# Performance work log

Hardware: AMD Instinct MI355X
Metric: run time of the kernel (lower is better)

The kernel has to match this reference:

```python
import jax, jax.numpy as jnp
import numpy as np

B, S, D = 4, 4096, 1024
H, EXPAND, DCONV = 8, 2, 4
DI = D * EXPAND           # d_inner = 2048
HD = DI // H              # head_dim = 256
LN_EPS = 1e-5


def setup_inputs() -> dict:
    key = jax.random.key(0)
    ks = jax.random.split(key, 6)
    scale = lambda fan_in: 1.0 / np.sqrt(fan_in)
    return {
        "x": jax.random.normal(ks[0], (B, S, D), dtype=jnp.float32),
        "norm_w": jnp.ones((D,), dtype=jnp.float32),
        "norm_b": jnp.zeros((D,), dtype=jnp.float32),
        "in_proj_w": jax.random.normal(ks[1], (2 * DI, D), dtype=jnp.float32) * scale(D),
        "conv_w": jax.random.normal(ks[2], (DI, 1, DCONV), dtype=jnp.float32) * scale(DCONV),
        "conv_b": jax.random.normal(ks[3], (DI,), dtype=jnp.float32) * 0.02,
        "out_proj_w": jax.random.normal(ks[4], (D, DI), dtype=jnp.float32) * scale(DI),
        "log_alpha": jax.random.uniform(ks[5], (H,), dtype=jnp.float32,
                                        minval=np.log(0.1), maxval=np.log(0.99)),
    }


def reference(x, norm_w, norm_b, in_proj_w, conv_w, conv_b, out_proj_w, log_alpha):
    residual = x
    # LayerNorm
    mu = jnp.mean(x, axis=-1, keepdims=True)
    var = jnp.var(x, axis=-1, keepdims=True)
    xn = (x - mu) * jax.lax.rsqrt(var + LN_EPS) * norm_w + norm_b
    # input projection -> [B, S, 2*DI]
    xz = jnp.einsum("bsd,ed->bse", xn, in_proj_w)
    x_path, gate = xz[..., :DI], xz[..., DI:]
    # causal depthwise conv1d (torch pads d_conv-1 both sides then slices [:S])
    kernel = jnp.transpose(conv_w, (2, 1, 0))  # [DCONV, 1, DI] (WIO)
    x_path = jax.lax.conv_general_dilated(
        x_path, kernel, window_strides=(1,), padding=[(DCONV - 1, 0)],
        dimension_numbers=("NWC", "WIO", "NWC"), feature_group_count=DI,
    ) + conv_b
    # multi-head scalar-decay linear recurrence: y_t = alpha*y_{t-1} + x_t
    xh = x_path.reshape(B, S, H, HD)
    alpha = jax.nn.sigmoid(log_alpha)[:, None]  # [H, 1]

    def step(y, xt):
        y = alpha * y + xt
        return y, y

    y0 = jnp.zeros((B, H, HD), dtype=x.dtype)
    _, ys = jax.lax.scan(step, y0, jnp.transpose(xh, (1, 0, 2, 3)))  # [S, B, H, HD]
    x_path = jnp.transpose(ys, (1, 0, 2, 3)).reshape(B, S, DI)
    # gate + output projection (dropout in eval mode = identity)
    x_path = jax.nn.silu(x_path) * gate
    out = jnp.einsum("bse,de->bsd", x_path, out_proj_w)
    return out + residual
```

## Files before the change

kernel.cpp:

```cpp
#include <hip/hip_runtime.h>
#include <hip/hip_bf16.h>
#include <cstdint>

#define Bb 4
#define Ss 4096
#define Dd 1024
#define Hh 8
#define DI 2048
#define HD 256
#define XZN 4096
#define Mtot 16384
#define NCH 128
#define CHUNK 32

typedef __bf16 bf16_t;
typedef __bf16 bf16x8 __attribute__((ext_vector_type(8)));
typedef __bf16 bf16x4 __attribute__((ext_vector_type(4)));
typedef float f32x4 __attribute__((ext_vector_type(4)));

__device__ __forceinline__ float sigmoidf_(float x) { return 1.f / (1.f + __expf(-x)); }

__device__ __forceinline__ void async_ld16(void* lds, const void* g) {
  __builtin_amdgcn_global_load_lds(
      (const __attribute__((address_space(1))) void*)(uintptr_t)g,
      (__attribute__((address_space(3))) void*)(uint32_t)(uintptr_t)lds,
      16, 0, 0);
}

__global__ __launch_bounds__(256) void cvt_kernel(const float* __restrict__ s,
                                                  bf16_t* __restrict__ d) {
  const int i = blockIdx.x * 256 + threadIdx.x;
  const float4 v = ((const float4*)s)[i];
  bf16_t* o = d + 4 * (size_t)i;
  o[0] = (bf16_t)v.x; o[1] = (bf16_t)v.y; o[2] = (bf16_t)v.z; o[3] = (bf16_t)v.w;
}

__global__ __launch_bounds__(256) void ln_kernel(const float* __restrict__ x,
                                                 const float* __restrict__ w,
                                                 const float* __restrict__ b,
                                                 bf16_t* __restrict__ xn) {
  __shared__ float red[8];
  const int row = blockIdx.x;
  const float4 v = ((const float4*)(x + (size_t)row * Dd))[threadIdx.x];
  float s  = v.x + v.y + v.z + v.w;
  float s2 = v.x * v.x + v.y * v.y + v.z * v.z + v.w * v.w;
  #pragma unroll
  for (int off = 32; off; off >>= 1) { s += __shfl_down(s, off); s2 += __shfl_down(s2, off); }
  const int wave = threadIdx.x >> 6, lane = threadIdx.x & 63;
  if (lane == 0) { red[wave * 2] = s; red[wave * 2 + 1] = s2; }
  __syncthreads();
  if (threadIdx.x == 0) {
    float S = 0.f, S2 = 0.f;
    for (int i = 0; i < 4; ++i) { S += red[i * 2]; S2 += red[i * 2 + 1]; }
    red[0] = S; red[1] = S2;
  }
  __syncthreads();
  const float mean = red[0] * (1.f / Dd);
  const float var  = red[1] * (1.f / Dd) - mean * mean;
  const float rstd = rsqrtf(var + 1e-5f);
  const float4 wv = ((const float4*)w)[threadIdx.x];
  const float4 bv = ((const float4*)b)[threadIdx.x];
  bf16_t* o = xn + (size_t)row * Dd + threadIdx.x * 4;
  o[0] = (bf16_t)((v.x - mean) * rstd * wv.x + bv.x);
  o[1] = (bf16_t)((v.y - mean) * rstd * wv.y + bv.y);
  o[2] = (bf16_t)((v.z - mean) * rstd * wv.z + bv.z);
  o[3] = (bf16_t)((v.w - mean) * rstd * wv.w + bv.w);
}

template <int ADD_RES, int MINW>
__global__ __launch_bounds__(256, MINW) void gemm_bt(const bf16_t* __restrict__ A,
                                                     const bf16_t* __restrict__ Bw,
                                                     void* __restrict__ Cv,
                                                     const float* __restrict__ res,
                                                     int M, int N, int K) {
  __shared__ __align__(16) bf16_t As[128 * 64];
  __shared__ __align__(16) bf16_t Bs[128 * 64];
  const int tid = threadIdx.x;
  const int wave = tid >> 6, lane = tid & 63;
  const int bm = blockIdx.y, bn = blockIdx.x;
  const int waveM = (wave >> 1) << 6;
  const int waveN = (wave & 1) << 6;

  f32x4 acc[4][4];
  #pragma unroll
  for (int i = 0; i < 4; ++i)
    #pragma unroll
    for (int j = 0; j < 4; ++j) acc[i][j] = (f32x4){0.f, 0.f, 0.f, 0.f};

  const int pr = lane >> 3;
  const int cg = (lane & 7) ^ pr;
  const bf16_t* Ag = A + (size_t)(bm * 128 + pr) * K + cg * 8;
  const bf16_t* Bg = Bw + (size_t)(bn * 128 + pr) * K + cg * 8;

  const int fr = lane & 15;
  const int fq = lane >> 4;

  for (int kt = 0; kt < K; kt += 64) {
    #pragma unroll
    for (int i = 0; i < 4; ++i) {
      const int ii = wave * 4 + i;
      async_ld16(&As[ii * 512], Ag + (size_t)(ii * 8) * K + kt);
      async_ld16(&Bs[ii * 512], Bg + (size_t)(ii * 8) * K + kt);
    }
    __syncthreads();
    #pragma unroll
    for (int ks = 0; ks < 2; ++ks) {
      bf16x8 af[4], bfv[4];
      #pragma unroll
      for (int mt = 0; mt < 4; ++mt) {
        const int row = waveM + mt * 16 + fr;
        const int p = (ks * 4 + fq) ^ (row & 7);
        af[mt] = *(const bf16x8*)&As[row * 64 + p * 8];
      }
      #pragma unroll
      for (int nt = 0; nt < 4; ++nt) {
        const int row = waveN + nt * 16 + fr;
        const int p = (ks * 4 + fq) ^ (row & 7);
        bfv[nt] = *(const bf16x8*)&Bs[row * 64 + p * 8];
      }
      #pragma unroll
      for (int mt = 0; mt < 4; ++mt)
        #pragma unroll
        for (int nt = 0; nt < 4; ++nt)
          acc[mt][nt] =
              __builtin_amdgcn_mfma_f32_16x16x32_bf16(af[mt], bfv[nt], acc[mt][nt], 0, 0, 0);
    }
    __syncthreads();
  }

  const int n0 = bn * 128 + waveN + fr;
  const int m0 = bm * 128 + waveM + fq * 4;
  #pragma unroll
  for (int mt = 0; mt < 4; ++mt)
    #pragma unroll
    for (int nt = 0; nt < 4; ++nt)
      #pragma unroll
      for (int r = 0; r < 4; ++r) {
        const size_t m = (size_t)(m0 + mt * 16 + r);
        const size_t n = (size_t)(n0 + nt * 16);
        if (ADD_RES)
          ((float*)Cv)[m * N + n] = acc[mt][nt][r] + res[m * N + n];
        else
          ((bf16_t*)Cv)[m * N + n] = (bf16_t)acc[mt][nt][r];
      }
}

__global__ __launch_bounds__(256) void scanA_kernel(const bf16_t* __restrict__ xz,
                                                    const float* __restrict__ conv_w,
                                                    const float* __restrict__ conv_b,
                                                    const float* __restrict__ log_alpha,
                                                    float* __restrict__ carry) {
  const int half  = blockIdx.x & 1;
  const int chunk = (blockIdx.x >> 1) & (NCH - 1);
  const int b     = blockIdx.x >> 8;
  const int ch    = half * 1024 + threadIdx.x * 4;
  const float alpha = sigmoidf_(log_alpha[ch >> 8]);
  float w[4][4], bias[4];
  #pragma unroll
  for (int j = 0; j < 4; ++j) {
    const float4 cw = ((const float4*)conv_w)[ch + j];
    w[j][0] = cw.x; w[j][1] = cw.y; w[j][2] = cw.z; w[j][3] = cw.w;
    bias[j] = conv_b[ch + j];
  }
  const int s0 = chunk * CHUNK;
  const size_t base = ((size_t)b * Ss + s0) * XZN + ch;
  float x3[4] = {0,0,0,0}, x2[4] = {0,0,0,0}, x1[4] = {0,0,0,0}, y[4] = {0,0,0,0};
  if (chunk > 0) {
    const bf16x4 v3 = *(const bf16x4*)(xz + base - 3 * (size_t)XZN);
    const bf16x4 v2 = *(const bf16x4*)(xz + base - 2 * (size_t)XZN);
    const bf16x4 v1 = *(const bf16x4*)(xz + base - 1 * (size_t)XZN);
    #pragma unroll
    for (int j = 0; j < 4; ++j) { x3[j] = (float)v3[j]; x2[j] = (float)v2[j]; x1[j] = (float)v1[j]; }
  }
  #pragma unroll 4
  for (int t = 0; t < CHUNK; ++t) {
    const bf16x4 v = *(const bf16x4*)(xz + base + (size_t)t * XZN);
    #pragma unroll
    for (int j = 0; j < 4; ++j) {
      const float xc = (float)v[j];
      const float cv = bias[j] + w[j][0] * x3[j] + w[j][1] * x2[j] + w[j][2] * x1[j] + w[j][3] * xc;
      x3[j] = x2[j]; x2[j] = x1[j]; x1[j] = xc;
      y[j] = fmaf(alpha, y[j], cv);
    }
  }
  *(float4*)(carry + ((size_t)b * NCH + chunk) * DI + ch) =
      make_float4(y[0], y[1], y[2], y[3]);
}

__global__ __launch_bounds__(256) void scanB_kernel(const float* __restrict__ carry,
                                                    float* __restrict__ carryin,
                                                    const float* __restrict__ log_alpha) {
  __shared__ float S[8][32];
  const int b   = blockIdx.x >> 6;
  const int chg = blockIdx.x & 63;
  const int cg  = threadIdx.x >> 5;
  const int chl = threadIdx.x & 31;
  const int ch  = chg * 32 + chl;
  const float alpha = sigmoidf_(log_alpha[ch >> 8]);
  const float lal  = log2f(alpha);
  const float aL   = exp2f((float)CHUNK * lal);
  const float aL16 = exp2f((float)(CHUNK * 16) * lal);
  const size_t base = ((size_t)b * NCH + cg * 16) * DI + ch;
  float v[16];
  #pragma unroll
  for (int i = 0; i < 16; ++i) v[i] = carry[base + (size_t)i * DI];
  float Sl = v[0];
  #pragma unroll
  for (int i = 1; i < 16; ++i) Sl = fmaf(aL, Sl, v[i]);
  S[cg][chl] = Sl;
  __syncthreads();
  float P = 0.f;
  for (int h = 0; h < cg; ++h) P = fmaf(aL16, P, S[h][chl]);
  #pragma unroll
  for (int i = 0; i < 16; ++i) {
    carryin[base + (size_t)i * DI] = P;
    P = fmaf(aL, P, v[i]);
  }
}

__global__ __launch_bounds__(256) void scanC_kernel(const bf16_t* __restrict__ xz,
                                                    const float* __restrict__ conv_w,
                                                    const float* __restrict__ conv_b,
                                                    const float* __restrict__ log_alpha,
                                                    const float* __restrict__ carryin,
                                                    bf16_t* __restrict__ act) {
  const int half  = blockIdx.x & 1;
  const int chunk = (blockIdx.x >> 1) & (NCH - 1);
  const int b     = blockIdx.x >> 8;
  const int ch    = half * 1024 + threadIdx.x * 4;
  const float alpha = sigmoidf_(log_alpha[ch >> 8]);
  float w[4][4], bias[4];
  #pragma unroll
  for (int j = 0; j < 4; ++j) {
    const float4 cw = ((const float4*)conv_w)[ch + j];
    w[j][0] = cw.x; w[j][1] = cw.y; w[j][2] = cw.z; w[j][3] = cw.w;
    bias[j] = conv_b[ch + j];
  }
  const int s0 = chunk * CHUNK;
  const size_t base = ((size_t)b * Ss + s0) * XZN + ch;
  float x3[4] = {0,0,0,0}, x2[4] = {0,0,0,0}, x1[4] = {0,0,0,0}, y[4];
  const float4 cin = *(const float4*)(carryin + ((size_t)b * NCH + chunk) * DI + ch);
  y[0] = cin.x; y[1] = cin.y; y[2] = cin.z; y[3] = cin.w;
  if (chunk > 0) {
    const bf16x4 v3 = *(const bf16x4*)(xz + base - 3 * (size_t)XZN);
    const bf16x4 v2 = *(const bf16x4*)(xz + base - 2 * (size_t)XZN);
    const bf16x4 v1 = *(const bf16x4*)(xz + base - 1 * (size_t)XZN);
    #pragma unroll
    for (int j = 0; j < 4; ++j) { x3[j] = (float)v3[j]; x2[j] = (float)v2[j]; x1[j] = (float)v1[j]; }
  }
  const size_t abase = ((size_t)b * Ss + s0) * DI + ch;
  #pragma unroll 4
  for (int t = 0; t < CHUNK; ++t) {
    const bf16x4 v = *(const bf16x4*)(xz + base + (size_t)t * XZN);
    const bf16x4 gv = *(const bf16x4*)(xz + base + (size_t)t * XZN + DI);
    bf16x4 ov;
    #pragma unroll
    for (int j = 0; j < 4; ++j) {
      const float xc = (float)v[j];
      const float cv = bias[j] + w[j][0] * x3[j] + w[j][1] * x2[j] + w[j][2] * x1[j] + w[j][3] * xc;
      x3[j] = x2[j]; x2[j] = x1[j]; x1[j] = xc;
      y[j] = fmaf(alpha, y[j], cv);
      const float o = y[j] * (1.f / (1.f + __expf(-y[j]))) * (float)gv[j];
      ov[j] = (bf16_t)o;
    }
    *(bf16x4*)(act + abase + (size_t)t * DI) = ov;
  }
}

extern "C" void kernel_launch(void* const* d_in, const int* in_sizes, int n_in,
                              void* d_out, int out_size, void* d_ws, size_t ws_size,
                              hipStream_t stream) {
  const float* x          = (const float*)d_in[0];
  const float* norm_w     = (const float*)d_in[1];
  const float* norm_b     = (const float*)d_in[2];
  const float* in_proj_w  = (const float*)d_in[3];
  const float* conv_w     = (const float*)d_in[4];
  const float* conv_b     = (const float*)d_in[5];
  const float* out_proj_w = (const float*)d_in[6];
  const float* log_alpha  = (const float*)d_in[7];
  float* out = (float*)d_out;

  char* ws = (char*)d_ws;
  bf16_t* xn     = (bf16_t*)(ws);
  bf16_t* w_in   = (bf16_t*)(ws + 33554432);
  bf16_t* w_out  = (bf16_t*)(ws + 41943040);
  bf16_t* xz     = (bf16_t*)(ws + 46137344);
  bf16_t* act    = (bf16_t*)(ws + 180355072);
  float*  carry   = (float*)(ws);
  float*  carryin = (float*)(ws + 4194304);

  cvt_kernel<<<4096, 256, 0, stream>>>(in_proj_w, w_in);
  cvt_kernel<<<2048, 256, 0, stream>>>(out_proj_w, w_out);
  ln_kernel<<<Mtot, 256, 0, stream>>>(x, norm_w, norm_b, xn);

  dim3 g1(XZN / 128, Mtot / 128);
  gemm_bt<0, 1><<<g1, 256, 0, stream>>>(xn, w_in, xz, nullptr, Mtot, XZN, Dd);

  scanA_kernel<<<Bb * NCH * 2, 256, 0, stream>>>(xz, conv_w, conv_b, log_alpha, carry);
  scanB_kernel<<<Bb * 64, 256, 0, stream>>>(carry, carryin, log_alpha);
  scanC_kernel<<<Bb * NCH * 2, 256, 0, stream>>>(xz, conv_w, conv_b, log_alpha, carryin, act);

  dim3 g2(Dd / 128, Mtot / 128);
  gemm_bt<1, 4><<<g2, 256, 0, stream>>>(act, w_out, out, x, Mtot, Dd, DI);
}
```

Measured before the change: 439.1 us.

## Replace GEMM with 256x256-tile, 4-stage async-pipelined kernel with block swizzle

Both projection GEMMs move from a 128x128 tile with a single-buffered LDS load and two barriers per K-step to a 256x256 tile run by 512 threads. The new kernel keeps a 4-deep ring of LDS buffers filled with async global-to-LDS loads, waits on vmcnt so loads overlap MFMA work, and raises wave priority around the MFMA block. Workgroup IDs are remapped so neighbouring tiles are spread across XCDs. The goals are better arithmetic intensity and hidden memory latency. The costs are a larger LDS footprint (64 KB), more accumulator registers per wave, and fewer workgroups for the smaller output GEMM (256 blocks).

```diff
diff --git a/kernel.cpp b/kernel.cpp
--- a/kernel.cpp
+++ b/kernel.cpp
@@ -67,71 +67,101 @@
   o[3] = (bf16_t)((v.w - mean) * rstd * wv.w + bv.w);
 }
 
-template <int ADD_RES, int MINW>
-__global__ __launch_bounds__(256, MINW) void gemm_bt(const bf16_t* __restrict__ A,
-                                                     const bf16_t* __restrict__ Bw,
-                                                     void* __restrict__ Cv,
-                                                     const float* __restrict__ res,
-                                                     int M, int N, int K) {
-  __shared__ __align__(16) bf16_t As[128 * 64];
-  __shared__ __align__(16) bf16_t Bs[128 * 64];
+template <int ADD_RES>
+__global__ __launch_bounds__(512, 2) void gemm256(const bf16_t* __restrict__ A,
+                                                  const bf16_t* __restrict__ Bw,
+                                                  void* __restrict__ Cv,
+                                                  const float* __restrict__ res,
+                                                  int M, int N, int K) {
+  __shared__ __align__(16) bf16_t As[4][8192];
+  __shared__ __align__(16) bf16_t Bs[4][8192];
   const int tid = threadIdx.x;
   const int wave = tid >> 6, lane = tid & 63;
-  const int bm = blockIdx.y, bn = blockIdx.x;
-  const int waveM = (wave >> 1) << 6;
-  const int waveN = (wave & 1) << 6;
-
-  f32x4 acc[4][4];
-  #pragma unroll
-  for (int i = 0; i < 4; ++i)
+  const int wm = wave >> 2, wn = wave & 3;
+
+  const int nbx = gridDim.x;
+  const int nwg = nbx * gridDim.y;
+  const int bid0 = blockIdx.y * nbx + blockIdx.x;
+  const int cpx = nwg >> 3;
+  const int bid = (bid0 & 7) * cpx + (bid0 >> 3);
+  const int bm = bid / nbx, bn = bid % nbx;
+
+  f32x4 acc[8][4];
+  #pragma unroll
+  for (int i = 0; i < 8; ++i)
     #pragma unroll
     for (int j = 0; j < 4; ++j) acc[i][j] = (f32x4){0.f, 0.f, 0.f, 0.f};
 
-  const int pr = lane >> 3;
-  const int cg = (lane & 7) ^ pr;
-  const bf16_t* Ag = A + (size_t)(bm * 128 + pr) * K + cg * 8;
-  const bf16_t* Bg = Bw + (size_t)(bn * 128 + pr) * K + cg * 8;
-
-  const int fr = lane & 15;
-  const int fq = lane >> 4;
-
-  for (int kt = 0; kt < K; kt += 64) {
-    #pragma unroll
-    for (int i = 0; i < 4; ++i) {
-      const int ii = wave * 4 + i;
-      async_ld16(&As[ii * 512], Ag + (size_t)(ii * 8) * K + kt);
-      async_ld16(&Bs[ii * 512], Bg + (size_t)(ii * 8) * K + kt);
+  const int srow = tid >> 2;
+  const int sc   = (tid & 3) ^ ((tid >> 3) & 3);
+  const bf16_t* Ag = A  + (size_t)(bm * 256 + srow) * K + sc * 8;
+  const bf16_t* Bg = Bw + (size_t)(bn * 256 + srow) * K + sc * 8;
+  const size_t rowK128 = (size_t)128 * K;
+  char* const AsB = (char*)As + (wave << 10);
+  char* const BsB = (char*)Bs + (wave << 10);
+
+  const int fr = lane & 15, fq = lane >> 4;
+  int aoff[8], boff[4];
+  #pragma unroll
+  for (int mt = 0; mt < 8; ++mt) {
+    const int row = wm * 128 + mt * 16 + fr;
+    aoff[mt] = row * 64 + ((fq ^ ((row >> 1) & 3)) << 4);
+  }
+  #pragma unroll
+  for (int nt = 0; nt < 4; ++nt) {
+    const int row = wn * 64 + nt * 16 + fr;
+    boff[nt] = row * 64 + ((fq ^ ((row >> 1) & 3)) << 4);
+  }
+
+  const int NT = K >> 5;
+  #pragma unroll
+  for (int t = 0; t < 3; ++t) {
+    const int kt = t << 5;
+    async_ld16(AsB + t * 16384,        Ag + kt);
+    async_ld16(AsB + t * 16384 + 8192, Ag + rowK128 + kt);
+    async_ld16(BsB + t * 16384,        Bg + kt);
+    async_ld16(BsB + t * 16384 + 8192, Bg + rowK128 + kt);
+  }
+
+  for (int t = 0; t < NT; ++t) {
+    const int rem = NT - 1 - t;
+    if (rem >= 2)      asm volatile("s_waitcnt vmcnt(8)" ::: "memory");
+    else if (rem == 1) asm volatile("s_waitcnt vmcnt(4)" ::: "memory");
+    else               asm volatile("s_waitcnt vmcnt(0)" ::: "memory");
+    __builtin_amdgcn_s_barrier();
+
+    const int buf = t & 3;
+    const char* Ab = (const char*)As + buf * 16384;
+    const char* Bbp = (const char*)Bs + buf * 16384;
+    bf16x8 af[8], bfv[4];
+    #pragma unroll
+    for (int mt = 0; mt < 8; ++mt) af[mt] = *(const bf16x8*)(Ab + aoff[mt]);
+    #pragma unroll
+    for (int nt = 0; nt < 4; ++nt) bfv[nt] = *(const bf16x8*)(Bbp + boff[nt]);
+
+    if (t + 3 < NT) {
+      const int b = (t + 3) & 3;
+      const int kt = (t + 3) << 5;
+      async_ld16(AsB + b * 16384,        Ag + kt);
+      async_ld16(AsB + b * 16384 + 8192, Ag + rowK128 + kt);
+      async_ld16(BsB + b * 16384,        Bg + kt);
+      async_ld16(BsB + b * 16384 + 8192, Bg + rowK128 + kt);
     }
-    __syncthreads();
-    #pragma unroll
-    for (int ks = 0; ks < 2; ++ks) {
-      bf16x8 af[4], bfv[4];
+
+    __builtin_amdgcn_s_setprio(1);
+    #pragma unroll
+    for (int mt = 0; mt < 8; ++mt)
       #pragma unroll
-      for (int mt = 0; mt < 4; ++mt) {
-        const int row = waveM + mt * 16 + fr;
-        const int p = (ks * 4 + fq) ^ (row & 7);
-        af[mt] = *(const bf16x8*)&As[row * 64 + p * 8];
-      }
-      #pragma unroll
-      for (int nt = 0; nt < 4; ++nt) {
-        const int row = waveN + nt * 16 + fr;
-        const int p = (ks * 4 + fq) ^ (row & 7);
-        bfv[nt] = *(const bf16x8*)&Bs[row * 64 + p * 8];
-      }
-      #pragma unroll
-      for (int mt = 0; mt < 4; ++mt)
-        #pragma unroll
-        for (int nt = 0; nt < 4; ++nt)
-          acc[mt][nt] =
-              __builtin_amdgcn_mfma_f32_16x16x32_bf16(af[mt], bfv[nt], acc[mt][nt], 0, 0, 0);
-    }
-    __syncthreads();
-  }
-
-  const int n0 = bn * 128 + waveN + fr;
-  const int m0 = bm * 128 + waveM + fq * 4;
-  #pragma unroll
-  for (int mt = 0; mt < 4; ++mt)
+      for (int nt = 0; nt < 4; ++nt)
+        acc[mt][nt] =
+            __builtin_amdgcn_mfma_f32_16x16x32_bf16(af[mt], bfv[nt], acc[mt][nt], 0, 0, 0);
+    __builtin_amdgcn_s_setprio(0);
+  }
+
+  const int m0 = bm * 256 + wm * 128 + fq * 4;
+  const int n0 = bn * 256 + wn * 64 + fr;
+  #pragma unroll
+  for (int mt = 0; mt < 8; ++mt)
     #pragma unroll
     for (int nt = 0; nt < 4; ++nt)
       #pragma unroll
@@ -293,13 +323,13 @@
   cvt_kernel<<<2048, 256, 0, stream>>>(out_proj_w, w_out);
   ln_kernel<<<Mtot, 256, 0, stream>>>(x, norm_w, norm_b, xn);
 
-  dim3 g1(XZN / 128, Mtot / 128);
-  gemm_bt<0, 1><<<g1, 256, 0, stream>>>(xn, w_in, xz, nullptr, Mtot, XZN, Dd);
+  dim3 g1(XZN / 256, Mtot / 256);
+  gemm256<0><<<g1, 512, 0, stream>>>(xn, w_in, xz, nullptr, Mtot, XZN, Dd);
 
   scanA_kernel<<<Bb * NCH * 2, 256, 0, stream>>>(xz, conv_w, conv_b, log_alpha, carry);
   scanB_kernel<<<Bb * 64, 256, 0, stream>>>(carry, carryin, log_alpha);
   scanC_kernel<<<Bb * NCH * 2, 256, 0, stream>>>(xz, conv_w, conv_b, log_alpha, carryin, act);
 
-  dim3 g2(Dd / 128, Mtot / 128);
-  gemm_bt<1, 4><<<g2, 256, 0, stream>>>(act, w_out, out, x, Mtot, Dd, DI);
-}
+  dim3 g2(Dd / 256, Mtot / 256);
+  gemm256<1><<<g2, 512, 0, stream>>>(act, w_out, out, x, Mtot, Dd, DI);
+}
```

Result: faster. 407.8 us (-7.1%).
